# Optimization experiments

Measured on AMD Instinct MI355X. Metric: run time of the kernel, lower is better.

## Reference

```python
import jax, jax.numpy as jnp
import numpy as np

HEADS = 8
DIM_HEAD = 64

def setup_inputs() -> dict:
    key = jax.random.key(0)
    k1, k2, k3 = jax.random.split(key, 3)
    B, L, D = 8, 4096, 512
    hidden = HEADS * DIM_HEAD  # 512
    x = jax.random.normal(k1, (B, L, D), dtype=jnp.float32)
    # Conv1d(kernel_size=1) weights, squeezed to 2D matrices
    Wqkv = jax.random.normal(k2, (3 * hidden, D), dtype=jnp.float32) * (1.0 / np.sqrt(D))
    Wout = jax.random.normal(k3, (D, hidden), dtype=jnp.float32) * (1.0 / np.sqrt(hidden))
    bout = jnp.zeros((D,), dtype=jnp.float32)
    return {"x": x, "Wqkv": Wqkv, "Wout": Wout, "bout": bout}

def reference(x, Wqkv, Wout, bout):
    B, L, D = x.shape
    H, C = HEADS, DIM_HEAD
    # pointwise conv == linear over channel dim: (b, 3*H*C, l)
    qkv = jnp.einsum('bld,od->bol', x, Wqkv)
    qkv = qkv.reshape(B, 3, H, C, L)  # channel split order: (qkv, heads, c)
    q, k, v = qkv[:, 0], qkv[:, 1], qkv[:, 2]  # each (b, h, c, l)
    k = jax.nn.softmax(k, axis=-1)   # softmax over sequence
    q = jax.nn.softmax(q, axis=-2)   # softmax over feature dim (q_norm=True)
    context = jnp.einsum('bhdn,bhen->bhde', k, v)   # (b,h,c,c)
    out = jnp.einsum('bhde,bhdn->bhen', context, q)  # (b,h,c,l)
    out = out.reshape(B, H * C, L)
    y = jnp.einsum('bcl,dc->bld', out, Wout) + bout  # to_out + permute back
    return y
```

## Files before the change

kernel.cpp:

```cpp
#include <hip/hip_runtime.h>

#define L 4096
#define D 512
#define NCH 16

typedef __bf16 bf16x8 __attribute__((ext_vector_type(8)));
typedef float  f32x4  __attribute__((ext_vector_type(4)));

__device__ __forceinline__ void load_lds16(const void* g, void* l) {
    __builtin_amdgcn_global_load_lds(
        (const __attribute__((address_space(1))) void*)g,
        (__attribute__((address_space(3))) void*)l, 16, 0, 0);
}

__device__ __forceinline__ void barrier_mem() {
    asm volatile("" ::: "memory");
    __builtin_amdgcn_s_barrier();
    asm volatile("" ::: "memory");
}

#define NX8  (8 * 4096 * 512 / 8)
#define NW18 (1536 * 512 / 8)
#define NW28 (512 * 512 / 8)
__global__ __launch_bounds__(256) void convert_all(const float* __restrict__ x,
                                                   const float* __restrict__ Wq,
                                                   const float* __restrict__ Wo,
                                                   __bf16* __restrict__ dst) {
    int i = blockIdx.x * 256 + threadIdx.x;
    if (i >= NX8 + NW18 + NW28) return;
    const float* s;
    if (i < NX8)             s = x  + (size_t)i * 8;
    else if (i < NX8 + NW18) s = Wq + (size_t)(i - NX8) * 8;
    else                     s = Wo + (size_t)(i - NX8 - NW18) * 8;
    float4 a = ((const float4*)s)[0], b = ((const float4*)s)[1];
    bf16x8 o = {(__bf16)a.x, (__bf16)a.y, (__bf16)a.z, (__bf16)a.w,
                (__bf16)b.x, (__bf16)b.y, (__bf16)b.z, (__bf16)b.w};
    *(bf16x8*)(dst + (size_t)i * 8) = o;
}

template <int M, int N, int K, typename CT>
__global__ __launch_bounds__(512, 2) void gemm_bf16_8ph(
    const __bf16* __restrict__ A, size_t aStride,
    const __bf16* __restrict__ B, size_t bStride,
    CT* __restrict__ C, size_t cStride,
    const float* __restrict__ bias) {
    __shared__ __align__(16) __bf16 sB[2][256 * 64];
    __shared__ __align__(16) __bf16 sA[2][256 * 64];
    constexpr int NT = K / 64;
    const int b  = blockIdx.z;
    const int m0 = blockIdx.y * 256;
    const int n0 = blockIdx.x * 256;
    const int t    = threadIdx.x;
    const int wave = t >> 6, lane = t & 63;
    const int wm = (wave >> 2) * 128;
    const int wn = (wave & 3) * 64;
    const int fr = lane & 15, g = lane >> 4;
    const __bf16* Ab = A + (size_t)b * aStride + (size_t)m0 * K;
    const __bf16* Bb = B + (size_t)b * bStride + (size_t)n0 * K;
    CT* Cb = C + (size_t)b * cStride;

    const __bf16* pA_[4];
    const __bf16* pB_[4];
#pragma unroll
    for (int k = 0; k < 4; ++k) {
        const int gi = k * 512 + t, row = gi >> 3, cc = gi & 7;
        pA_[k] = Ab + (size_t)row * K + (cc ^ (row & 7)) * 8;
        pB_[k] = Bb + (size_t)row * K + (cc ^ (row & 7)) * 8;
    }
    const int lc0 = ((0 + g) ^ (fr & 7)) * 8;
    const int lc1 = ((4 + g) ^ (fr & 7)) * 8;

    f32x4 acc[8][4];
#pragma unroll
    for (int i = 0; i < 8; i++)
#pragma unroll
        for (int j = 0; j < 4; j++) acc[i][j] = (f32x4)(0.0f);

    auto stageH = [&](int kt, int pb, int h) {
#pragma unroll
        for (int k = h * 2; k < h * 2 + 2; ++k) {
            load_lds16(pA_[k] + kt * 64, &sA[pb][(k * 512 + t) * 8]);
            load_lds16(pB_[k] + kt * 64, &sB[pb][(k * 512 + t) * 8]);
        }
    };

    stageH(0, 0, 0);
    stageH(0, 0, 1);

    bf16x8 fB[4], fA[4];
#pragma unroll
    for (int kt = 0; kt < NT; ++kt) {
        const int p = kt & 1;
        if (kt + 1 < NT) {
            stageH(kt + 1, p ^ 1, 0);
            asm volatile("s_waitcnt vmcnt(4)" ::: "memory");
        } else {
            asm volatile("s_waitcnt vmcnt(0)" ::: "memory");
        }
        barrier_mem();
#pragma unroll
        for (int j = 0; j < 4; ++j)
            fB[j] = *(const bf16x8*)&sB[p][(wn + j * 16 + fr) * 64 + lc0];
#pragma unroll
        for (int i = 0; i < 4; ++i)
            fA[i] = *(const bf16x8*)&sA[p][(wm + i * 16 + fr) * 64 + lc0];
        asm volatile("s_waitcnt lgkmcnt(0)" ::: "memory");
        __builtin_amdgcn_sched_barrier(0);
        __builtin_amdgcn_s_setprio(1);
#pragma unroll
        for (int i = 0; i < 4; ++i)
#pragma unroll
            for (int j = 0; j < 4; ++j)
                acc[i][j] = __builtin_amdgcn_mfma_f32_16x16x32_bf16(fA[i], fB[j], acc[i][j], 0, 0, 0);
        __builtin_amdgcn_s_setprio(0);
        barrier_mem();
#pragma unroll
        for (int i = 0; i < 4; ++i)
            fA[i] = *(const bf16x8*)&sA[p][(wm + 64 + i * 16 + fr) * 64 + lc0];
        if (kt + 1 < NT) stageH(kt + 1, p ^ 1, 1);
        barrier_mem();
        asm volatile("s_waitcnt lgkmcnt(0)" ::: "memory");
        __builtin_amdgcn_sched_barrier(0);
        __builtin_amdgcn_s_setprio(1);
#pragma unroll
        for (int i = 0; i < 4; ++i)
#pragma unroll
            for (int j = 0; j < 4; ++j)
                acc[4 + i][j] = __builtin_amdgcn_mfma_f32_16x16x32_bf16(fA[i], fB[j], acc[4 + i][j], 0, 0, 0);
        __builtin_amdgcn_s_setprio(0);
        barrier_mem();
#pragma unroll
        for (int j = 0; j < 4; ++j)
            fB[j] = *(const bf16x8*)&sB[p][(wn + j * 16 + fr) * 64 + lc1];
#pragma unroll
        for (int i = 0; i < 4; ++i)
            fA[i] = *(const bf16x8*)&sA[p][(wm + i * 16 + fr) * 64 + lc1];
        barrier_mem();
        asm volatile("s_waitcnt lgkmcnt(0)" ::: "memory");
        __builtin_amdgcn_sched_barrier(0);
        __builtin_amdgcn_s_setprio(1);
#pragma unroll
        for (int i = 0; i < 4; ++i)
#pragma unroll
            for (int j = 0; j < 4; ++j)
                acc[i][j] = __builtin_amdgcn_mfma_f32_16x16x32_bf16(fA[i], fB[j], acc[i][j], 0, 0, 0);
        __builtin_amdgcn_s_setprio(0);
        barrier_mem();
#pragma unroll
        for (int i = 0; i < 4; ++i)
            fA[i] = *(const bf16x8*)&sA[p][(wm + 64 + i * 16 + fr) * 64 + lc1];
        barrier_mem();
        asm volatile("s_waitcnt lgkmcnt(0)" ::: "memory");
        __builtin_amdgcn_sched_barrier(0);
        __builtin_amdgcn_s_setprio(1);
#pragma unroll
        for (int i = 0; i < 4; ++i)
#pragma unroll
            for (int j = 0; j < 4; ++j)
                acc[4 + i][j] = __builtin_amdgcn_mfma_f32_16x16x32_bf16(fA[i], fB[j], acc[4 + i][j], 0, 0, 0);
        __builtin_amdgcn_s_setprio(0);
        barrier_mem();
    }

    const int rb = g * 4;
    float bv[4];
#pragma unroll
    for (int j = 0; j < 4; ++j) bv[j] = bias ? bias[n0 + wn + j * 16 + fr] : 0.0f;
#pragma unroll
    for (int i = 0; i < 8; ++i) {
#pragma unroll
        for (int r = 0; r < 4; ++r) {
            const int m = m0 + wm + i * 16 + rb + r;
            CT* rowp = Cb + (size_t)m * N + n0 + wn + fr;
#pragma unroll
            for (int j = 0; j < 4; ++j)
                rowp[j * 16] = (CT)(acc[i][j][r] + bv[j]);
        }
    }
}

__global__ __launch_bounds__(256) void kstats(const __bf16* __restrict__ qkv,
                                              float2* __restrict__ stats) {
    const int r = blockIdx.x;
    const int b = r >> 9, hc = r & 511;
    const __bf16* row = qkv + (size_t)b * 1536 * L + (size_t)(512 + hc) * L;
    __shared__ float sred[4];
    const int t = threadIdx.x;
    const bf16x8* p = (const bf16x8*)row;
    bf16x8 c0 = p[t * 2], c1 = p[t * 2 + 1];
    float v[16];
    float m = -1e30f;
#pragma unroll
    for (int j = 0; j < 8; j++) {
        v[j] = (float)c0[j];
        v[8 + j] = (float)c1[j];
    }
#pragma unroll
    for (int j = 0; j < 16; j++) m = fmaxf(m, v[j]);
#pragma unroll
    for (int off = 32; off > 0; off >>= 1) m = fmaxf(m, __shfl_down(m, off, 64));
    if ((t & 63) == 0) sred[t >> 6] = m;
    __syncthreads();
    const float m4 = fmaxf(fmaxf(sred[0], sred[1]), fmaxf(sred[2], sred[3]));
    float s = 0.f;
#pragma unroll
    for (int j = 0; j < 16; j++) s += __expf(v[j] - m4);
#pragma unroll
    for (int off = 32; off > 0; off >>= 1) s += __shfl_down(s, off, 64);
    __syncthreads();
    if ((t & 63) == 0) sred[t >> 6] = s;
    __syncthreads();
    if (t == 0) {
        const float stot = sred[0] + sred[1] + sred[2] + sred[3];
        stats[r] = make_float2(m4, 1.0f / stot);
    }
}

#define SKS 264
__global__ __launch_bounds__(256) void context_mfma(const __bf16* __restrict__ qkv,
                                                    const float2* __restrict__ stats,
                                                    float* __restrict__ ctxp) {
    __shared__ __align__(16) __bf16 smem[2 * 64 * SKS];
    __shared__ float smax[64];
    __bf16* sk = smem;
    __bf16* sv = smem + 64 * SKS;
    const int chunk = blockIdx.x;
    const int bh = blockIdx.y;
    const int b = bh >> 3, h = bh & 7;
    const __bf16* kbase = qkv + (size_t)b * 1536 * L + (size_t)(512 + h * 64) * L;
    const __bf16* vbase = qkv + (size_t)b * 1536 * L + (size_t)(1024 + h * 64) * L;
    const int t = threadIdx.x;
    if (t < 64) smax[t] = stats[bh * 64 + t].x;
    __syncthreads();

    {
        const int d = t >> 2, noff = (t & 3) * 64;
        const int n0 = chunk * 256;
        const __bf16* kp = kbase + (size_t)d * L + n0 + noff;
        const __bf16* vp = vbase + (size_t)d * L + n0 + noff;
        const float md = smax[d];
#pragma unroll
        for (int c = 0; c < 8; c++) {
            bf16x8 kk = *(const bf16x8*)(kp + c * 8);
            bf16x8 vv = *(const bf16x8*)(vp + c * 8);
            bf16x8 ek;
#pragma unroll
            for (int j = 0; j < 8; j++) ek[j] = (__bf16)__expf((float)kk[j] - md);
            *(bf16x8*)&sk[d * SKS + noff + c * 8] = ek;
            *(bf16x8*)&sv[d * SKS + noff + c * 8] = vv;
        }
    }
    __syncthreads();

    const int wave = t >> 6, lane = t & 63;
    const int fr = lane & 15, kq = (lane >> 4) * 8;
    f32x4 acc[4][4];
#pragma unroll
    for (int i = 0; i < 4; i++)
#pragma unroll
        for (int j = 0; j < 4; j++) acc[i][j] = (f32x4)(0.0f);
#pragma unroll
    for (int kh = 0; kh < 2; kh++) {
        const int koff = wave * 64 + kh * 32 + kq;
        bf16x8 af[4], bfr[4];
#pragma unroll
        for (int i = 0; i < 4; i++) {
            af[i]  = *(const bf16x8*)&sk[(i * 16 + fr) * SKS + koff];
            bfr[i] = *(const bf16x8*)&sv[(i * 16 + fr) * SKS + koff];
        }
#pragma unroll
        for (int i = 0; i < 4; i++)
#pragma unroll
            for (int j = 0; j < 4; j++)
                acc[i][j] = __builtin_amdgcn_mfma_f32_16x16x32_bf16(af[i], bfr[j], acc[i][j], 0, 0, 0);
    }
    __syncthreads();

    float* red = (float*)smem;
    const int col = lane & 15, rbase = (lane >> 4) * 4;
#pragma unroll
    for (int i = 0; i < 4; i++)
#pragma unroll
        for (int j = 0; j < 4; j++)
#pragma unroll
            for (int r = 0; r < 4; r++) {
                const int dd = i * 16 + rbase + r;
                const int ee = j * 16 + col;
                red[wave * 4096 + dd * 64 + ee] = acc[i][j][r];
            }
    __syncthreads();
    float* cp = ctxp + ((size_t)chunk * 64 + bh) * 4096;
#pragma unroll
    for (int gg = 0; gg < 4; gg++) {
        const int idx = t * 16 + gg * 4;
        f32x4 s = *(const f32x4*)&red[idx];
        s += *(const f32x4*)&red[4096 + idx];
        s += *(const f32x4*)&red[8192 + idx];
        s += *(const f32x4*)&red[12288 + idx];
        *(f32x4*)&cp[idx] = s;
    }
}

__global__ __launch_bounds__(256) void ctx_reduce(const float* __restrict__ ctxp,
                                                  const float2* __restrict__ stats,
                                                  __bf16* __restrict__ ctxT) {
    const int bh = blockIdx.x >> 2, quarter = blockIdx.x & 3;
    const int t = threadIdx.x;
    const int flat = quarter * 1024 + t * 4;
    const int d = flat >> 6, e0 = flat & 63;
    f32x4 s = (f32x4)(0.0f);
    for (int ch = 0; ch < NCH; ch++)
        s += *(const f32x4*)&ctxp[((size_t)ch * 64 + bh) * 4096 + flat];
    const float inv = stats[bh * 64 + d].y;
    __bf16* o = ctxT + (size_t)bh * 4096;
#pragma unroll
    for (int j = 0; j < 4; j++) o[(e0 + j) * 64 + d] = (__bf16)(s[j] * inv);
}

#define SPS 66
__global__ __launch_bounds__(256) void pv_fused(__bf16* __restrict__ qkv,
                                                const __bf16* __restrict__ ctxT) {
    __shared__ __align__(16) __bf16 sp[256 * SPS];
    __shared__ __align__(16) __bf16 sctx[64 * SPS];
    __shared__ float sinv[256];
    const int tileN = blockIdx.x;
    const int bh = blockIdx.y;
    const int b = bh >> 3, h = bh & 7;
    const int t = threadIdx.x;
    const int n0 = tileN * 256;
    const __bf16* qbase = qkv + (size_t)b * 1536 * L + (size_t)(h * 64) * L;

    {
        const int e = t >> 2, c = t & 3;
        const bf16x8* src = (const bf16x8*)(ctxT + ((size_t)bh * 64 + e) * 64 + c * 16);
        *(bf16x8*)&sctx[e * SPS + c * 16] = src[0];
        *(bf16x8*)&sctx[e * SPS + c * 16 + 8] = src[1];
    }

    float m = -1e30f;
    float qv[64];
#pragma unroll
    for (int d = 0; d < 64; d++) {
        qv[d] = (float)qbase[(size_t)d * L + n0 + t];
        m = fmaxf(m, qv[d]);
    }
    float s = 0.f;
#pragma unroll
    for (int d0 = 0; d0 < 64; d0 += 8) {
        bf16x8 ek;
#pragma unroll
        for (int j = 0; j < 8; j++) {
            float e = __expf(qv[d0 + j] - m);
            s += e;
            ek[j] = (__bf16)e;
        }
        *(bf16x8*)&sp[t * SPS + d0] = ek;
    }
    sinv[t] = 1.0f / s;
    __syncthreads();

    const int wave = t >> 6, lane = t & 63;
    const int wm = wave * 64;
    const int fr = lane & 15, kq = (lane >> 4) * 8;
    f32x4 acc[4][4];
#pragma unroll
    for (int i = 0; i < 4; i++)
#pragma unroll
        for (int j = 0; j < 4; j++) acc[i][j] = (f32x4)(0.0f);
#pragma unroll
    for (int kh = 0; kh < 2; kh++) {
        bf16x8 af[4], bfr[4];
#pragma unroll
        for (int i = 0; i < 4; i++)
            af[i] = *(const bf16x8*)&sp[(wm + i * 16 + fr) * SPS + kh * 32 + kq];
#pragma unroll
        for (int j = 0; j < 4; j++)
            bfr[j] = *(const bf16x8*)&sctx[(j * 16 + fr) * SPS + kh * 32 + kq];
#pragma unroll
        for (int i = 0; i < 4; i++)
#pragma unroll
            for (int j = 0; j < 4; j++)
                acc[i][j] = __builtin_amdgcn_mfma_f32_16x16x32_bf16(af[i], bfr[j], acc[i][j], 0, 0, 0);
    }

    __bf16* ob = qkv + (size_t)b * 1536 * L + (size_t)512 * L;
    const int col = lane & 15, rbase = (lane >> 4) * 4;
#pragma unroll
    for (int i = 0; i < 4; i++) {
#pragma unroll
        for (int r = 0; r < 4; r++) {
            const int nl = wm + i * 16 + rbase + r;
            const float inv = sinv[nl];
            const size_t rowoff = (size_t)(n0 + nl) * 512 + h * 64;
#pragma unroll
            for (int j = 0; j < 4; j++)
                ob[rowoff + j * 16 + col] = (__bf16)(acc[i][j][r] * inv);
        }
    }
}

extern "C" void kernel_launch(void* const* d_in, const int* in_sizes, int n_in,
                              void* d_out, int out_size, void* d_ws, size_t ws_size,
                              hipStream_t stream) {
    const float* x    = (const float*)d_in[0];
    const float* Wqkv = (const float*)d_in[1];
    const float* Wout = (const float*)d_in[2];
    const float* bout = (const float*)d_in[3];
    float* y = (float*)d_out;

    __bf16* qkv   = (__bf16*)d_ws;
    float*  ctxp  = (float*)(qkv + (size_t)8 * 1536 * L);
    __bf16* xb    = (__bf16*)(ctxp + (size_t)NCH * 64 * 4096);
    __bf16* Wqb   = xb + (size_t)8 * 4096 * 512;
    __bf16* Wob   = Wqb + (size_t)1536 * 512;
    float2* stats = (float2*)(Wob + (size_t)512 * 512);
    __bf16* ctxT  = (__bf16*)(stats + 4096);

    const int convBlocks = (NX8 + NW18 + NW28 + 255) / 256;
    convert_all<<<dim3(convBlocks), 256, 0, stream>>>(x, Wqkv, Wout, xb);

    gemm_bf16_8ph<1536, 4096, 512, __bf16><<<dim3(4096 / 256, 1536 / 256, 8), 512, 0, stream>>>(
        Wqb, 0, xb, (size_t)4096 * 512, qkv, (size_t)1536 * 4096, nullptr);

    kstats<<<dim3(4096), 256, 0, stream>>>(qkv, stats);
    context_mfma<<<dim3(NCH, 64), 256, 0, stream>>>(qkv, stats, ctxp);
    ctx_reduce<<<dim3(256), 256, 0, stream>>>(ctxp, stats, ctxT);
    pv_fused<<<dim3(L / 256, 64), 256, 0, stream>>>(qkv, ctxT);

    const __bf16* outT = qkv + (size_t)512 * L;
    gemm_bf16_8ph<4096, 512, 512, float><<<dim3(512 / 256, 4096 / 256, 8), 512, 0, stream>>>(
        outT, (size_t)1536 * L, Wob, 0, y, (size_t)4096 * 512, bout);
}
```

Baseline: 266.3 us.

## Fuse key softmax stats and context reduction into context kernel via online softmax

Removes the separate kstats pass over K and the ctx_reduce launch. Each context block now computes per-chunk max and sum of its K slice and writes them along with its partial context. The last block to finish each head, found through an atomic counter, rescales the partials with flash-style max correction and writes the normalized transposed context. This saves one full read of K and two kernel launches. In exchange it adds atomics and thread fences, a serial tail for the last block per head, and counter resets placed inside the convert kernel.

After: 470.7 us. +76.8%, slower.

```diff
diff --git a/kernel.cpp b/kernel.cpp
--- a/kernel.cpp
+++ b/kernel.cpp
@@ -25,7 +25,9 @@
 __global__ __launch_bounds__(256) void convert_all(const float* __restrict__ x,
                                                    const float* __restrict__ Wq,
                                                    const float* __restrict__ Wo,
-                                                   __bf16* __restrict__ dst) {
+                                                   __bf16* __restrict__ dst,
+                                                   int* __restrict__ cnt) {
+    if (blockIdx.x == 0 && threadIdx.x < 64) cnt[threadIdx.x] = 0;
     int i = blockIdx.x * 256 + threadIdx.x;
     if (i >= NX8 + NW18 + NW28) return;
     const float* s;
@@ -179,49 +181,15 @@
     }
 }
 
-__global__ __launch_bounds__(256) void kstats(const __bf16* __restrict__ qkv,
-                                              float2* __restrict__ stats) {
-    const int r = blockIdx.x;
-    const int b = r >> 9, hc = r & 511;
-    const __bf16* row = qkv + (size_t)b * 1536 * L + (size_t)(512 + hc) * L;
-    __shared__ float sred[4];
-    const int t = threadIdx.x;
-    const bf16x8* p = (const bf16x8*)row;
-    bf16x8 c0 = p[t * 2], c1 = p[t * 2 + 1];
-    float v[16];
-    float m = -1e30f;
-#pragma unroll
-    for (int j = 0; j < 8; j++) {
-        v[j] = (float)c0[j];
-        v[8 + j] = (float)c1[j];
-    }
-#pragma unroll
-    for (int j = 0; j < 16; j++) m = fmaxf(m, v[j]);
-#pragma unroll
-    for (int off = 32; off > 0; off >>= 1) m = fmaxf(m, __shfl_down(m, off, 64));
-    if ((t & 63) == 0) sred[t >> 6] = m;
-    __syncthreads();
-    const float m4 = fmaxf(fmaxf(sred[0], sred[1]), fmaxf(sred[2], sred[3]));
-    float s = 0.f;
-#pragma unroll
-    for (int j = 0; j < 16; j++) s += __expf(v[j] - m4);
-#pragma unroll
-    for (int off = 32; off > 0; off >>= 1) s += __shfl_down(s, off, 64);
-    __syncthreads();
-    if ((t & 63) == 0) sred[t >> 6] = s;
-    __syncthreads();
-    if (t == 0) {
-        const float stot = sred[0] + sred[1] + sred[2] + sred[3];
-        stats[r] = make_float2(m4, 1.0f / stot);
-    }
-}
-
 #define SKS 264
-__global__ __launch_bounds__(256) void context_mfma(const __bf16* __restrict__ qkv,
-                                                    const float2* __restrict__ stats,
-                                                    float* __restrict__ ctxp) {
+__global__ __launch_bounds__(256) void context_fused(const __bf16* __restrict__ qkv,
+                                                     float* __restrict__ ctxp,
+                                                     float* __restrict__ mstat,
+                                                     float* __restrict__ sstat,
+                                                     int* __restrict__ cnt,
+                                                     __bf16* __restrict__ ctxT) {
     __shared__ __align__(16) __bf16 smem[2 * 64 * SKS];
-    __shared__ float smax[64];
+    __shared__ int isLast;
     __bf16* sk = smem;
     __bf16* sv = smem + 64 * SKS;
     const int chunk = blockIdx.x;
@@ -230,24 +198,41 @@
     const __bf16* kbase = qkv + (size_t)b * 1536 * L + (size_t)(512 + h * 64) * L;
     const __bf16* vbase = qkv + (size_t)b * 1536 * L + (size_t)(1024 + h * 64) * L;
     const int t = threadIdx.x;
-    if (t < 64) smax[t] = stats[bh * 64 + t].x;
-    __syncthreads();
 
     {
         const int d = t >> 2, noff = (t & 3) * 64;
         const int n0 = chunk * 256;
         const __bf16* kp = kbase + (size_t)d * L + n0 + noff;
         const __bf16* vp = vbase + (size_t)d * L + n0 + noff;
-        const float md = smax[d];
+        bf16x8 kk[8];
+        float m = -1e30f;
 #pragma unroll
         for (int c = 0; c < 8; c++) {
-            bf16x8 kk = *(const bf16x8*)(kp + c * 8);
+            kk[c] = *(const bf16x8*)(kp + c * 8);
             bf16x8 vv = *(const bf16x8*)(vp + c * 8);
+            *(bf16x8*)&sv[d * SKS + noff + c * 8] = vv;
+#pragma unroll
+            for (int j = 0; j < 8; j++) m = fmaxf(m, (float)kk[c][j]);
+        }
+        m = fmaxf(m, __shfl_xor(m, 1, 64));
+        m = fmaxf(m, __shfl_xor(m, 2, 64));
+        float s = 0.f;
+#pragma unroll
+        for (int c = 0; c < 8; c++) {
             bf16x8 ek;
 #pragma unroll
-            for (int j = 0; j < 8; j++) ek[j] = (__bf16)__expf((float)kk[j] - md);
+            for (int j = 0; j < 8; j++) {
+                float e = __expf((float)kk[c][j] - m);
+                s += e;
+                ek[j] = (__bf16)e;
+            }
             *(bf16x8*)&sk[d * SKS + noff + c * 8] = ek;
-            *(bf16x8*)&sv[d * SKS + noff + c * 8] = vv;
+        }
+        s += __shfl_xor(s, 1, 64);
+        s += __shfl_xor(s, 2, 64);
+        if ((t & 3) == 0) {
+            mstat[((size_t)chunk * 64 + bh) * 64 + d] = m;
+            sstat[((size_t)chunk * 64 + bh) * 64 + d] = s;
         }
     }
     __syncthreads();
@@ -299,22 +284,45 @@
         s += *(const f32x4*)&red[12288 + idx];
         *(f32x4*)&cp[idx] = s;
     }
-}
-
-__global__ __launch_bounds__(256) void ctx_reduce(const float* __restrict__ ctxp,
-                                                  const float2* __restrict__ stats,
-                                                  __bf16* __restrict__ ctxT) {
-    const int bh = blockIdx.x >> 2, quarter = blockIdx.x & 3;
-    const int t = threadIdx.x;
-    const int flat = quarter * 1024 + t * 4;
-    const int d = flat >> 6, e0 = flat & 63;
-    f32x4 s = (f32x4)(0.0f);
+
+    __threadfence();
+    if (t == 0) isLast = (atomicAdd(&cnt[bh], 1) == NCH - 1);
+    __syncthreads();
+    if (!isLast) return;
+    __threadfence();
+
+    const int rd = t >> 2;
+    const int re0 = (t & 3) * 16;
+    float M = -1e30f;
+#pragma unroll
     for (int ch = 0; ch < NCH; ch++)
-        s += *(const f32x4*)&ctxp[((size_t)ch * 64 + bh) * 4096 + flat];
-    const float inv = stats[bh * 64 + d].y;
+        M = fmaxf(M, mstat[((size_t)ch * 64 + bh) * 64 + rd]);
+    float S = 0.f;
+    float w[NCH];
+#pragma unroll
+    for (int ch = 0; ch < NCH; ch++) {
+        w[ch] = __expf(mstat[((size_t)ch * 64 + bh) * 64 + rd] - M);
+        S += sstat[((size_t)ch * 64 + bh) * 64 + rd] * w[ch];
+    }
+    const float inv = 1.0f / S;
+    f32x4 a4[4];
+#pragma unroll
+    for (int k = 0; k < 4; k++) a4[k] = (f32x4)(0.0f);
+#pragma unroll
+    for (int ch = 0; ch < NCH; ch++) {
+        const float* pc = ctxp + ((size_t)ch * 64 + bh) * 4096 + rd * 64 + re0;
+#pragma unroll
+        for (int k = 0; k < 4; k++) {
+            f32x4 v = *(const f32x4*)&pc[k * 4];
+            a4[k] += v * w[ch];
+        }
+    }
     __bf16* o = ctxT + (size_t)bh * 4096;
 #pragma unroll
-    for (int j = 0; j < 4; j++) o[(e0 + j) * 64 + d] = (__bf16)(s[j] * inv);
+    for (int k = 0; k < 4; k++)
+#pragma unroll
+        for (int j = 0; j < 4; j++)
+            o[(re0 + k * 4 + j) * 64 + rd] = (__bf16)(a4[k][j] * inv);
 }
 
 #define SPS 66
@@ -413,18 +421,18 @@
     __bf16* xb    = (__bf16*)(ctxp + (size_t)NCH * 64 * 4096);
     __bf16* Wqb   = xb + (size_t)8 * 4096 * 512;
     __bf16* Wob   = Wqb + (size_t)1536 * 512;
-    float2* stats = (float2*)(Wob + (size_t)512 * 512);
-    __bf16* ctxT  = (__bf16*)(stats + 4096);
+    float*  mstat = (float*)(Wob + (size_t)512 * 512);
+    float*  sstat = mstat + (size_t)NCH * 64 * 64;
+    int*    cnt   = (int*)(sstat + (size_t)NCH * 64 * 64);
+    __bf16* ctxT  = (__bf16*)(cnt + 64);
 
     const int convBlocks = (NX8 + NW18 + NW28 + 255) / 256;
-    convert_all<<<dim3(convBlocks), 256, 0, stream>>>(x, Wqkv, Wout, xb);
+    convert_all<<<dim3(convBlocks), 256, 0, stream>>>(x, Wqkv, Wout, xb, cnt);
 
     gemm_bf16_8ph<1536, 4096, 512, __bf16><<<dim3(4096 / 256, 1536 / 256, 8), 512, 0, stream>>>(
         Wqb, 0, xb, (size_t)4096 * 512, qkv, (size_t)1536 * 4096, nullptr);
 
-    kstats<<<dim3(4096), 256, 0, stream>>>(qkv, stats);
-    context_mfma<<<dim3(NCH, 64), 256, 0, stream>>>(qkv, stats, ctxp);
-    ctx_reduce<<<dim3(256), 256, 0, stream>>>(ctxp, stats, ctxT);
+    context_fused<<<dim3(NCH, 64), 256, 0, stream>>>(qkv, ctxp, mstat, sstat, cnt, ctxT);
     pv_fused<<<dim3(L / 256, 64), 256, 0, stream>>>(qkv, ctxT);
 
     const __bf16* outT = qkv + (size_t)512 * L;
```
